# Optimization experiments

Hardware: AMD Instinct MI355X
Metric: run time of the kernel (lower is better)

The kernel has to match this reference:

```python
import jax, jax.numpy as jnp
import numpy as np

N_WIDTH = 64
N_ORDER = 4
N_ELEMENTS = 250
N_NODES = N_ELEMENTS * N_ORDER + 1
N_COLL = 200
NDIM = 2
X_MIN = 0.0
X_MAX = 1.0
M = N_ORDER + 1  # nodes per element


def _bases(x):
    # x: [B, W, D] local coords in [-1, 1]; returns phi/dphi/ddphi as [B, W, M, D]
    nodes = jnp.linspace(-1.0, 1.0, M)
    eye = jnp.eye(M, dtype=bool)
    ne = ~eye
    diff = nodes[:, None] - nodes[None, :]
    inv = jnp.where(eye, 0.0, 1.0 / jnp.where(eye, 1.0, diff))  # inv[j,m] = 1/(n_j - n_m)
    r = (x[..., None, None] - nodes) * inv  # [B,W,D,j,m] = (x - n_m)/(n_j - n_m)
    # Lagrange values: L_j = prod_{m != j} r[j,m]
    L = jnp.prod(jnp.where(ne, r, 1.0), axis=-1)  # [B,W,D,M]
    # First derivative: dL_j = sum_{i != j} 1/(n_j-n_i) prod_{m != i,j} r[j,m]
    mask3 = ne[:, None, :] & ne[None, :, :]  # [j,i,m]: m!=j and m!=i
    P = jnp.prod(jnp.where(mask3, r[..., :, None, :], 1.0), axis=-1)  # [B,W,D,j,i]
    dL = jnp.sum(jnp.where(ne, inv, 0.0) * P, axis=-1)  # [B,W,D,M]
    # Faithful to the original indentation bug in dlagrange: the write
    # `dp_list[:, :, j, h] = y` sits OUTSIDE the j-loop, so only the last
    # column j = M-1 is ever filled; all other columns stay zero.
    dL = jnp.where(jnp.arange(M) == M - 1, dL, 0.0)
    # Second derivative: ddL_j = sum_{i!=j} 1/(n_j-n_i) sum_{m!=i,j} 1/(n_j-n_m) prod_{n!=i,j,m} r[j,n]
    mask4 = ne[:, None, None, :] & ne[None, :, None, :] & ne[None, None, :, :]  # [j,i,m,n]
    prodn = jnp.prod(jnp.where(mask4, r[..., :, None, None, :], 1.0), axis=-1)  # [B,W,D,j,i,m]
    Kprod = inv[:, None, :] * prodn
    Ksum = jnp.sum(jnp.where(mask3, Kprod, 0.0), axis=-1)  # [B,W,D,j,i]
    ddL = jnp.sum(jnp.where(ne, inv, 0.0) * Ksum, axis=-1)  # [B,W,D,M]
    tr = lambda a: jnp.transpose(a, (0, 1, 3, 2))  # -> [B,W,M,D]
    return tr(L), tr(dL), tr(ddL)


def _scatter(x, sample, phi_buf, dphi_buf, ddphi_buf):
    B = x.shape[0]
    xr = jnp.broadcast_to(x[:, None, :], (B, N_WIDTH, NDIM))
    x_shift = (N_NODES - 1) * (xr - X_MIN) / (X_MAX - X_MIN)
    id_el = jnp.clip(jnp.floor(x_shift / N_ORDER), 0, N_ELEMENTS - 1)
    nl = (id_el * N_ORDER).astype(jnp.int32)
    nr = nl + N_ORDER
    xt = (x_shift - 0.5 * (nl + nr)) / (0.5 * (nr - nl))
    dx = 0.5 * N_ORDER * (X_MAX - X_MIN) / (N_NODES - 1)
    phi_l, dphi_l, ddphi_l = _bases(xt)
    # Faithful quirk: the torch code indexes nodes_in_l[0, layer], a length-D
    # vector, so each (layer, node, dim-column) scalar is written at the node
    # offsets of ALL input dims.
    Lidx = nl[0]  # [W, D]
    wr = jnp.arange(N_WIDTH)
    for d in range(NDIM):
        for p in range(M):
            v = phi_l[0, :, p, d]
            dv = dphi_l[0, :, p, d] / dx
            ddv = ddphi_l[0, :, p, d] / (dx * dx)
            for dq in range(NDIM):
                pos = Lidx[:, dq] + p
                phi_buf = phi_buf.at[sample, wr, pos, d].set(v)
                dphi_buf = dphi_buf.at[sample, wr, pos, d].set(dv)
                ddphi_buf = ddphi_buf.at[sample, wr, pos, d].set(ddv)
    return phi_buf, dphi_buf, ddphi_buf, dx


def reference(x, flag, sample, weight, phi_buf, dphi_buf, ddphi_buf):
    if flag == 0:
        phi_buf, dphi_buf, ddphi_buf, dx = _scatter(x, sample, phi_buf, dphi_buf, ddphi_buf)
    else:
        dx = 0.5 * N_ORDER * (X_MAX - X_MIN) / (N_NODES - 1)
    # torch.no_grad() on the cuts -> stop_gradient
    phi_cut = jax.lax.stop_gradient(phi_buf[sample:sample + 1])
    dphi_cut = jax.lax.stop_gradient(dphi_buf[sample:sample + 1])
    ddphi_cut = jax.lax.stop_gradient(ddphi_buf[sample:sample + 1])
    t_ik = jnp.einsum('kpj,ikpj->ik', weight, phi_cut)
    dt_ik = jnp.einsum('kpj,ikpj->ik', weight, dphi_cut)
    ddt_ik = jnp.einsum('kpj,ikpj->ik', weight, ddphi_cut)
    return (t_ik, dt_ik, ddt_ik, phi_buf, dphi_buf, ddphi_buf)


def setup_inputs() -> dict:
    key = jax.random.key(0)
    k1, k2 = jax.random.split(key)
    x = jax.random.uniform(k1, (1, NDIM), dtype=jnp.float32)
    weight = jax.random.normal(k2, (N_WIDTH, N_NODES, NDIM), dtype=jnp.float32)
    zeros = lambda: jnp.zeros((N_COLL, N_WIDTH, N_NODES, NDIM), dtype=jnp.float32)
    return {
        'x': x,
        'flag': 0,
        'sample': 7,
        'weight': weight,
        'phi_buf': zeros(),
        'dphi_buf': zeros(),
        'ddphi_buf': zeros(),
    }
```

## Files before the change

### kernel.cpp

```cpp
#include <hip/hip_runtime.h>

#define N_WIDTH 64
#define N_ORDER 4
#define N_ELEMENTS 250
#define N_NODES 1001
#define N_COLL 200
#define NDIM 2
#define MM 5
#define ROW (N_NODES * NDIM)
#define SAMPLE_SLICE (N_WIDTH * ROW)
#define BUF_ELEMS ((long)N_COLL * SAMPLE_SLICE)
#define BLOCKS_PER_BUF 2048

typedef float v4f __attribute__((ext_vector_type(4)));

__global__ void copy_seg_kernel(const v4f* __restrict__ a, v4f* __restrict__ oa,
                                const v4f* __restrict__ b, v4f* __restrict__ ob,
                                const v4f* __restrict__ c, v4f* __restrict__ oc,
                                long n4) {
    int buf = blockIdx.x / BLOCKS_PER_BUF;
    int bid = blockIdx.x % BLOCKS_PER_BUF;
    const v4f* __restrict__ src = (buf == 0) ? a : (buf == 1) ? b : c;
    v4f* __restrict__ dst       = (buf == 0) ? oa : (buf == 1) ? ob : oc;
    long i = (long)bid * blockDim.x + threadIdx.x;
    long stride = (long)BLOCKS_PER_BUF * blockDim.x;
    for (; i < n4; i += stride) {
        v4f v = __builtin_nontemporal_load(&src[i]);
        __builtin_nontemporal_store(v, &dst[i]);
    }
}

__device__ __forceinline__ float wave_reduce(float v) {
    for (int off = 32; off > 0; off >>= 1) v += __shfl_down(v, off, 64);
    return v;
}

__global__ void scatter_reduce_kernel(const float* __restrict__ x,
                                      const int* __restrict__ flagp,
                                      const int* __restrict__ samplep,
                                      const float* __restrict__ weight,
                                      const float* __restrict__ phi_in,
                                      const float* __restrict__ dphi_in,
                                      const float* __restrict__ ddphi_in,
                                      float* __restrict__ phi_out,
                                      float* __restrict__ dphi_out,
                                      float* __restrict__ ddphi_out,
                                      float* __restrict__ t_out) {
    int k = blockIdx.x;
    int tid = threadIdx.x;
    int flag = *flagp;
    int sample = *samplep;
    long wbase = (long)k * ROW;
    long inbase = (long)sample * SAMPLE_SLICE + (long)k * ROW;

    float st = 0.0f, sdt = 0.0f, sddt = 0.0f;
    for (int i = tid; i < ROW; i += 256) {
        float wv = weight[wbase + i];
        st   += wv * phi_in[inbase + i];
        sdt  += wv * dphi_in[inbase + i];
        sddt += wv * ddphi_in[inbase + i];
    }

    if (flag == 0 && tid < NDIM) {
        int d = tid;
        float xs[NDIM];
        int nl[NDIM];
        for (int q = 0; q < NDIM; ++q) {
            xs[q] = (float)(N_NODES - 1) * x[q];
            float id_el = floorf(xs[q] / (float)N_ORDER);
            id_el = fminf(fmaxf(id_el, 0.0f), (float)(N_ELEMENTS - 1));
            nl[q] = (int)(id_el * (float)N_ORDER);
        }
        float xt = (xs[d] - ((float)nl[d] + 2.0f)) * 0.5f;

        const float nodes[MM] = {-1.0f, -0.5f, 0.0f, 0.5f, 1.0f};
        float inv[MM][MM], r[MM][MM];
        for (int i = 0; i < MM; ++i)
            for (int kk = 0; kk < MM; ++kk) {
                inv[i][kk] = (i == kk) ? 0.0f : 1.0f / (nodes[i] - nodes[kk]);
                r[i][kk] = (xt - nodes[kk]) * inv[i][kk];
            }

        float L[MM], dL[MM], ddL[MM];
        for (int i = 0; i < MM; ++i) {
            float prod = 1.0f;
            for (int kk = 0; kk < MM; ++kk) if (kk != i) prod *= r[i][kk];
            L[i] = prod;

            float s = 0.0f;
            for (int j = 0; j < MM; ++j) if (j != i) {
                float pr = 1.0f;
                for (int kk = 0; kk < MM; ++kk) if (kk != i && kk != j) pr *= r[i][kk];
                s += inv[i][j] * pr;
            }
            dL[i] = (i == MM - 1) ? s : 0.0f;

            float ss = 0.0f;
            for (int j = 0; j < MM; ++j) if (j != i) {
                float s2 = 0.0f;
                for (int kk = 0; kk < MM; ++kk) if (kk != i && kk != j) {
                    float pr = 1.0f;
                    for (int l = 0; l < MM; ++l) if (l != i && l != j && l != kk) pr *= r[i][l];
                    s2 += inv[i][kk] * pr;
                }
                ss += inv[i][j] * s2;
            }
            ddL[i] = ss;
        }

        const float dx = 0.5f * (float)N_ORDER / (float)(N_NODES - 1);
        const float inv_dx = 1.0f / dx;
        const float inv_dx2 = inv_dx * inv_dx;

        int qmin = min(nl[0], nl[1]);
        int qmax = max(nl[0], nl[1]) + N_ORDER;
        for (int q = qmin; q <= qmax; ++q) {
            int p0 = q - nl[0];
            int p1 = q - nl[1];
            int p = -1;
            if (p0 >= 0 && p0 <= N_ORDER) p = p0;
            if (p1 >= 0 && p1 <= N_ORDER && p1 > p) p = p1;
            if (p < 0) continue;
            float v   = L[p];
            float dv  = dL[p] * inv_dx;
            float ddv = ddL[p] * inv_dx2;
            long off = (long)q * NDIM + d;
            phi_out[inbase - wbase + wbase + off] = v;
            dphi_out[inbase + off - wbase + wbase] = dv;
            ddphi_out[inbase + off] = ddv;
            phi_out[inbase + off] = v;
            dphi_out[inbase + off] = dv;
            float wv = weight[wbase + off];
            st   += wv * (v   - phi_in[inbase + off]);
            sdt  += wv * (dv  - dphi_in[inbase + off]);
            sddt += wv * (ddv - ddphi_in[inbase + off]);
        }
    }

    st = wave_reduce(st);
    sdt = wave_reduce(sdt);
    sddt = wave_reduce(sddt);

    __shared__ float sh[3][4];
    int lane = tid & 63;
    int wid = tid >> 6;
    if (lane == 0) { sh[0][wid] = st; sh[1][wid] = sdt; sh[2][wid] = sddt; }
    __syncthreads();
    if (tid == 0) {
        t_out[k]       = sh[0][0] + sh[0][1] + sh[0][2] + sh[0][3];
        t_out[64 + k]  = sh[1][0] + sh[1][1] + sh[1][2] + sh[1][3];
        t_out[128 + k] = sh[2][0] + sh[2][1] + sh[2][2] + sh[2][3];
    }
}

extern "C" void kernel_launch(void* const* d_in, const int* in_sizes, int n_in,
                              void* d_out, int out_size, void* d_ws, size_t ws_size,
                              hipStream_t stream) {
    const float* x        = (const float*)d_in[0];
    const int*   flagp    = (const int*)d_in[1];
    const int*   samplep  = (const int*)d_in[2];
    const float* weight   = (const float*)d_in[3];
    const float* phi_in   = (const float*)d_in[4];
    const float* dphi_in  = (const float*)d_in[5];
    const float* ddphi_in = (const float*)d_in[6];

    float* out = (float*)d_out;
    float* t_out     = out;
    float* phi_out   = out + 192;
    float* dphi_out  = phi_out + BUF_ELEMS;
    float* ddphi_out = dphi_out + BUF_ELEMS;

    long n4 = BUF_ELEMS / 4;

    copy_seg_kernel<<<3 * BLOCKS_PER_BUF, 256, 0, stream>>>(
        (const v4f*)phi_in,  (v4f*)phi_out,
        (const v4f*)dphi_in, (v4f*)dphi_out,
        (const v4f*)ddphi_in,(v4f*)ddphi_out, n4);

    scatter_reduce_kernel<<<64, 256, 0, stream>>>(
        x, flagp, samplep, weight, phi_in, dphi_in, ddphi_in,
        phi_out, dphi_out, ddphi_out, t_out);
}
```

Measured before the change: 530.1 us.

## Fuse buffer copy and scatter-reduce into a single kernel launch

Merges the bulk copy kernel and the scatter/reduce kernel into one launch. Copy blocks skip the sampled slice, and 64 extra blocks rewrite that slice with the updated basis values while reducing against the weights. This removes one launch and the ordering dependency between the two kernels. The copy now uses plain float4 loads and stores instead of nontemporal ones, and interleaves all three buffers in a single loop.

Result: faster. 514.0 us (-3.0%).

```diff
diff --git a/kernel.cpp b/kernel.cpp
--- a/kernel.cpp
+++ b/kernel.cpp
@@ -9,83 +9,79 @@
 #define MM 5
 #define ROW (N_NODES * NDIM)
 #define SAMPLE_SLICE (N_WIDTH * ROW)
+#define SLICE4 (SAMPLE_SLICE / 4)
 #define BUF_ELEMS ((long)N_COLL * SAMPLE_SLICE)
-#define BLOCKS_PER_BUF 2048
-
-typedef float v4f __attribute__((ext_vector_type(4)));
-
-__global__ void copy_seg_kernel(const v4f* __restrict__ a, v4f* __restrict__ oa,
-                                const v4f* __restrict__ b, v4f* __restrict__ ob,
-                                const v4f* __restrict__ c, v4f* __restrict__ oc,
-                                long n4) {
-    int buf = blockIdx.x / BLOCKS_PER_BUF;
-    int bid = blockIdx.x % BLOCKS_PER_BUF;
-    const v4f* __restrict__ src = (buf == 0) ? a : (buf == 1) ? b : c;
-    v4f* __restrict__ dst       = (buf == 0) ? oa : (buf == 1) ? ob : oc;
-    long i = (long)bid * blockDim.x + threadIdx.x;
-    long stride = (long)BLOCKS_PER_BUF * blockDim.x;
-    for (; i < n4; i += stride) {
-        v4f v = __builtin_nontemporal_load(&src[i]);
-        __builtin_nontemporal_store(v, &dst[i]);
-    }
-}
+#define COPY_BLOCKS 2048
+#define RED_BLOCKS 64
 
 __device__ __forceinline__ float wave_reduce(float v) {
     for (int off = 32; off > 0; off >>= 1) v += __shfl_down(v, off, 64);
     return v;
 }
 
-__global__ void scatter_reduce_kernel(const float* __restrict__ x,
-                                      const int* __restrict__ flagp,
-                                      const int* __restrict__ samplep,
-                                      const float* __restrict__ weight,
-                                      const float* __restrict__ phi_in,
-                                      const float* __restrict__ dphi_in,
-                                      const float* __restrict__ ddphi_in,
-                                      float* __restrict__ phi_out,
-                                      float* __restrict__ dphi_out,
-                                      float* __restrict__ ddphi_out,
-                                      float* __restrict__ t_out) {
-    int k = blockIdx.x;
-    int tid = threadIdx.x;
-    int flag = *flagp;
-    int sample = *samplep;
-    long wbase = (long)k * ROW;
-    long inbase = (long)sample * SAMPLE_SLICE + (long)k * ROW;
+__global__ void fused_kernel(const float* __restrict__ x,
+                             const int* __restrict__ flagp,
+                             const int* __restrict__ samplep,
+                             const float* __restrict__ weight,
+                             const float* __restrict__ phi_in,
+                             const float* __restrict__ dphi_in,
+                             const float* __restrict__ ddphi_in,
+                             float* __restrict__ phi_out,
+                             float* __restrict__ dphi_out,
+                             float* __restrict__ ddphi_out,
+                             float* __restrict__ t_out) {
+    const int sample = *samplep;
+    const int tid = threadIdx.x;
 
-    float st = 0.0f, sdt = 0.0f, sddt = 0.0f;
-    for (int i = tid; i < ROW; i += 256) {
-        float wv = weight[wbase + i];
-        st   += wv * phi_in[inbase + i];
-        sdt  += wv * dphi_in[inbase + i];
-        sddt += wv * ddphi_in[inbase + i];
+    if (blockIdx.x < COPY_BLOCKS) {
+        const long skip_lo = (long)sample * SLICE4;
+        const long skip_hi = skip_lo + SLICE4;
+        const float4* __restrict__ a = (const float4*)phi_in;
+        const float4* __restrict__ b = (const float4*)dphi_in;
+        const float4* __restrict__ c = (const float4*)ddphi_in;
+        float4* __restrict__ oa = (float4*)phi_out;
+        float4* __restrict__ ob = (float4*)dphi_out;
+        float4* __restrict__ oc = (float4*)ddphi_out;
+        const long n4 = BUF_ELEMS / 4;
+        long i = (long)blockIdx.x * 256 + tid;
+        const long stride = (long)COPY_BLOCKS * 256;
+        for (; i < n4; i += stride) {
+            if (i >= skip_lo && i < skip_hi) continue;
+            oa[i] = a[i];
+            ob[i] = b[i];
+            oc[i] = c[i];
+        }
+        return;
     }
 
-    if (flag == 0 && tid < NDIM) {
-        int d = tid;
-        float xs[NDIM];
-        int nl[NDIM];
-        for (int q = 0; q < NDIM; ++q) {
-            xs[q] = (float)(N_NODES - 1) * x[q];
-            float id_el = floorf(xs[q] / (float)N_ORDER);
-            id_el = fminf(fmaxf(id_el, 0.0f), (float)(N_ELEMENTS - 1));
-            nl[q] = (int)(id_el * (float)N_ORDER);
-        }
+    const int k = blockIdx.x - COPY_BLOCKS;
+    const int flag = *flagp;
+    const long wbase = (long)k * ROW;
+    const long base = (long)sample * SAMPLE_SLICE + wbase;
+
+    float xs[NDIM];
+    int nl[NDIM];
+    for (int q = 0; q < NDIM; ++q) {
+        xs[q] = (float)(N_NODES - 1) * x[q];
+        float id_el = floorf(xs[q] / (float)N_ORDER);
+        id_el = fminf(fmaxf(id_el, 0.0f), (float)(N_ELEMENTS - 1));
+        nl[q] = (int)(id_el * (float)N_ORDER);
+    }
+
+    const float nodes[MM] = {-1.0f, -0.5f, 0.0f, 0.5f, 1.0f};
+    float L[NDIM][MM], dLv[NDIM][MM], ddLv[NDIM][MM];
+    for (int d = 0; d < NDIM; ++d) {
         float xt = (xs[d] - ((float)nl[d] + 2.0f)) * 0.5f;
-
-        const float nodes[MM] = {-1.0f, -0.5f, 0.0f, 0.5f, 1.0f};
         float inv[MM][MM], r[MM][MM];
         for (int i = 0; i < MM; ++i)
             for (int kk = 0; kk < MM; ++kk) {
                 inv[i][kk] = (i == kk) ? 0.0f : 1.0f / (nodes[i] - nodes[kk]);
                 r[i][kk] = (xt - nodes[kk]) * inv[i][kk];
             }
-
-        float L[MM], dL[MM], ddL[MM];
         for (int i = 0; i < MM; ++i) {
             float prod = 1.0f;
             for (int kk = 0; kk < MM; ++kk) if (kk != i) prod *= r[i][kk];
-            L[i] = prod;
+            L[d][i] = prod;
 
             float s = 0.0f;
             for (int j = 0; j < MM; ++j) if (j != i) {
@@ -93,7 +89,7 @@
                 for (int kk = 0; kk < MM; ++kk) if (kk != i && kk != j) pr *= r[i][kk];
                 s += inv[i][j] * pr;
             }
-            dL[i] = (i == MM - 1) ? s : 0.0f;
+            dLv[d][i] = (i == MM - 1) ? s : 0.0f;
 
             float ss = 0.0f;
             for (int j = 0; j < MM; ++j) if (j != i) {
@@ -105,36 +101,40 @@
                 }
                 ss += inv[i][j] * s2;
             }
-            ddL[i] = ss;
+            ddLv[d][i] = ss;
         }
+    }
 
-        const float dx = 0.5f * (float)N_ORDER / (float)(N_NODES - 1);
-        const float inv_dx = 1.0f / dx;
-        const float inv_dx2 = inv_dx * inv_dx;
+    const float dx = 0.5f * (float)N_ORDER / (float)(N_NODES - 1);
+    const float inv_dx = 1.0f / dx;
+    const float inv_dx2 = inv_dx * inv_dx;
 
-        int qmin = min(nl[0], nl[1]);
-        int qmax = max(nl[0], nl[1]) + N_ORDER;
-        for (int q = qmin; q <= qmax; ++q) {
+    float st = 0.0f, sdt = 0.0f, sddt = 0.0f;
+    for (int i = tid; i < ROW; i += 256) {
+        float v   = phi_in[base + i];
+        float dv  = dphi_in[base + i];
+        float ddv = ddphi_in[base + i];
+        if (flag == 0) {
+            int q = i >> 1;
+            int d = i & 1;
             int p0 = q - nl[0];
             int p1 = q - nl[1];
             int p = -1;
             if (p0 >= 0 && p0 <= N_ORDER) p = p0;
             if (p1 >= 0 && p1 <= N_ORDER && p1 > p) p = p1;
-            if (p < 0) continue;
-            float v   = L[p];
-            float dv  = dL[p] * inv_dx;
-            float ddv = ddL[p] * inv_dx2;
-            long off = (long)q * NDIM + d;
-            phi_out[inbase - wbase + wbase + off] = v;
-            dphi_out[inbase + off - wbase + wbase] = dv;
-            ddphi_out[inbase + off] = ddv;
-            phi_out[inbase + off] = v;
-            dphi_out[inbase + off] = dv;
-            float wv = weight[wbase + off];
-            st   += wv * (v   - phi_in[inbase + off]);
-            sdt  += wv * (dv  - dphi_in[inbase + off]);
-            sddt += wv * (ddv - ddphi_in[inbase + off]);
+            if (p >= 0) {
+                v   = L[d][p];
+                dv  = dLv[d][p] * inv_dx;
+                ddv = ddLv[d][p] * inv_dx2;
+            }
         }
+        phi_out[base + i]   = v;
+        dphi_out[base + i]  = dv;
+        ddphi_out[base + i] = ddv;
+        float wv = weight[wbase + i];
+        st   += wv * v;
+        sdt  += wv * dv;
+        sddt += wv * ddv;
     }
 
     st = wave_reduce(st);
@@ -170,14 +170,7 @@
     float* dphi_out  = phi_out + BUF_ELEMS;
     float* ddphi_out = dphi_out + BUF_ELEMS;
 
-    long n4 = BUF_ELEMS / 4;
-
-    copy_seg_kernel<<<3 * BLOCKS_PER_BUF, 256, 0, stream>>>(
-        (const v4f*)phi_in,  (v4f*)phi_out,
-        (const v4f*)dphi_in, (v4f*)dphi_out,
-        (const v4f*)ddphi_in,(v4f*)ddphi_out, n4);
-
-    scatter_reduce_kernel<<<64, 256, 0, stream>>>(
+    fused_kernel<<<COPY_BLOCKS + RED_BLOCKS, 256, 0, stream>>>(
         x, flagp, samplep, weight, phi_in, dphi_in, ddphi_in,
         phi_out, dphi_out, ddphi_out, t_out);
 }
```
